# Optimization experiments

Measured on AMD Instinct MI355X. Metric: run time of the kernel, lower is better.

Reference implementation:

```python
import jax, jax.numpy as jnp
import numpy as np

N = 8192
D = 128
NUM_CLASSES = 1000
MARGIN = 1.0
EPS = 1e-6  # torch.nn.functional.pairwise_distance default eps
FMAX = float(np.finfo(np.float32).max)


def setup_inputs() -> dict:
    key = jax.random.key(0)
    k_e, k_l = jax.random.split(key)
    embed = jax.random.normal(k_e, (N, D), dtype=jnp.float32)
    labels = jax.random.randint(k_l, (N,), 0, NUM_CLASSES, dtype=jnp.int64)
    return {"embed": embed, "labels": labels}


def reference(embed, labels):
    # Pairwise squared-L2 distance matrix: ||xi||^2 - 2 xi.xj + ||xj||^2  -> [N, N]
    norm_sq = jnp.sum(embed * embed, axis=1, keepdims=True)  # [N, 1]
    dist = norm_sq - 2.0 * (embed @ embed.T) + norm_sq.T     # [N, N]

    # Label similarity mask (int in original; float here for the multiplies)
    sim = (labels[:, None] == labels[None, :]).astype(dist.dtype)  # [N, N]

    # Hardest positive: argmax of masked distances
    hardest_pos = jnp.argmax(dist * sim, axis=1)  # [N]

    # Hardest negative: argmin over negatives, sentinel-replacing masked-out entries
    neg_masked = dist * (1.0 - sim)
    hardest_neg = jnp.argmin(neg_masked + (neg_masked <= 0).astype(dist.dtype) * FMAX, axis=1)

    a = embed
    p = embed[hardest_pos]  # [N, D]
    n = embed[hardest_neg]  # [N, D]

    # torch.nn.TripletMarginLoss(margin=MARGIN): mean(relu(d(a,p) - d(a,n) + margin))
    # with d(x, y) = ||x - y + eps||_2 (torch pairwise_distance semantics)
    d_ap = jnp.sqrt(jnp.sum((a - p + EPS) ** 2, axis=1))
    d_an = jnp.sqrt(jnp.sum((a - n + EPS) ** 2, axis=1))
    loss = jnp.mean(jnp.maximum(d_ap - d_an + MARGIN, 0.0))
    return loss
```

## Files before the change

### kernel.cpp

```cpp
#include <hip/hip_runtime.h>
#include <cstdint>

typedef unsigned long long u64;
typedef _Float16 half8 __attribute__((ext_vector_type(8)));
typedef float f32x4 __attribute__((ext_vector_type(4)));

static constexpr int Dd = 128;
static constexpr float EPSf = 1e-6f;
static constexpr float MARGINf = 1.0f;
static constexpr float BIGf = 3.0e38f;

__device__ __forceinline__ unsigned fkey(float f) {
  unsigned b = __float_as_uint(f);
  return (b & 0x80000000u) ? ~b : (b | 0x80000000u);
}

__global__ __launch_bounds__(256) void k_prep(const float* __restrict__ E,
                                              _Float16* __restrict__ Ehp,
                                              float* __restrict__ normf) {
  __shared__ float part[4][16];
  const int t = threadIdx.x;
  const int b = blockIdx.x;
  const int ks = t >> 6, r15 = t & 15;
  const int lg = (t >> 4) & 3;
  const float* src = E + (size_t)(b * 16 + r15) * Dd + ks * 32 + lg * 8;
  float4 v0 = *(const float4*)src;
  float4 v1 = *(const float4*)(src + 4);
  half8 hv;
  hv[0] = (_Float16)v0.x; hv[1] = (_Float16)v0.y;
  hv[2] = (_Float16)v0.z; hv[3] = (_Float16)v0.w;
  hv[4] = (_Float16)v1.x; hv[5] = (_Float16)v1.y;
  hv[6] = (_Float16)v1.z; hv[7] = (_Float16)v1.w;
  *(half8*)((char*)Ehp + (size_t)b * 4096 + t * 16) = hv;
  float s = v0.x * v0.x + v0.y * v0.y + v0.z * v0.z + v0.w * v0.w +
            v1.x * v1.x + v1.y * v1.y + v1.z * v1.z + v1.w * v1.w;
  s += __shfl_xor(s, 16);
  s += __shfl_xor(s, 32);
  if (((t >> 4) & 3) == 0) part[ks][r15] = s;
  __syncthreads();
  if (t < 16) normf[b * 16 + t] = part[0][t] + part[1][t] + part[2][t] + part[3][t];
}

__global__ __launch_bounds__(256, 3) void k_gemm(const _Float16* __restrict__ Ehp,
                                                 const float* __restrict__ normf,
                                                 const int* __restrict__ lab,
                                                 u64* __restrict__ posPart,
                                                 u64* __restrict__ negPart) {
  __shared__ __align__(16) char Jb[2][16384];
  __shared__ __align__(16) float njs[1024];
  __shared__ __align__(16) int ljs[1024];

  const int t = threadIdx.x;
  const int w = t >> 6, l = t & 63;
  const int lane15 = l & 15, lg = l >> 4;
  const int iw = w & 1, jw = w >> 1;
  const int panel = blockIdx.x;
  const int strip = blockIdx.y;
  const int ibase = panel * 128;
  const int jbase = strip * 1024;
  const char* jsrc = (const char*)Ehp + (size_t)(jbase >> 4) * 4096;

  #pragma unroll
  for (int q = 0; q < 4; ++q)
    *(half8*)(Jb[0] + q * 4096 + t * 16) = *(const half8*)(jsrc + q * 4096 + t * 16);
  *(float4*)&njs[t * 4] = *(const float4*)&normf[jbase + t * 4];
  *(int4*)&ljs[t * 4] = *(const int4*)&lab[jbase + t * 4];

  const int gi0 = ibase + iw * 64;
  half8 bf[4][4];
  #pragma unroll
  for (int it = 0; it < 4; ++it)
    #pragma unroll
    for (int ks = 0; ks < 4; ++ks)
      bf[it][ks] = *(const half8*)(Ehp + ((size_t)((gi0 >> 4) + it) * 4 + ks) * 512 +
                                   (size_t)l * 8);
  int li[4];
  #pragma unroll
  for (int it = 0; it < 4; ++it) li[it] = lab[gi0 + it * 16 + lane15];
  __syncthreads();

  float bp[4] = {-BIGf, -BIGf, -BIGf, -BIGf};
  float bn[4] = {BIGf, BIGf, BIGf, BIGf};

  for (int tile = 0; tile < 16; ++tile) {
    const int cur = tile & 1;
    half8 sreg[4];
    if (tile < 15) {
      const char* s = jsrc + (size_t)(tile + 1) * 16384;
      #pragma unroll
      for (int q = 0; q < 4; ++q) sreg[q] = *(const half8*)(s + q * 4096 + t * 16);
    }

    f32x4 acc[2][4];
    #pragma unroll
    for (int a = 0; a < 2; ++a)
      #pragma unroll
      for (int b = 0; b < 4; ++b) acc[a][b] = (f32x4){0.f, 0.f, 0.f, 0.f};

    #pragma unroll
    for (int ks = 0; ks < 4; ++ks) {
      half8 aj[2];
      #pragma unroll
      for (int jt = 0; jt < 2; ++jt)
        aj[jt] = *(const half8*)(Jb[cur] + ((jw * 2 + jt) * 4 + ks) * 1024 + l * 16);
      __builtin_amdgcn_s_setprio(1);
      #pragma unroll
      for (int jt = 0; jt < 2; ++jt)
        #pragma unroll
        for (int it = 0; it < 4; ++it)
          acc[jt][it] = __builtin_amdgcn_mfma_f32_16x16x32_f16(aj[jt], bf[it][ks], acc[jt][it], 0, 0, 0);
      __builtin_amdgcn_s_setprio(0);
    }

    #pragma unroll
    for (int jt = 0; jt < 2; ++jt) {
      const int jr0 = tile * 64 + jw * 32 + jt * 16 + lg * 4;
      const float4 nj4 = *(const float4*)&njs[jr0];
      const int4 lj4 = *(const int4*)&ljs[jr0];
      #pragma unroll
      for (int it = 0; it < 4; ++it) {
        float c0 = fmaf(acc[jt][it][0], -2.0f, nj4.x);
        float c1 = fmaf(acc[jt][it][1], -2.0f, nj4.y);
        float c2 = fmaf(acc[jt][it][2], -2.0f, nj4.z);
        float c3 = fmaf(acc[jt][it][3], -2.0f, nj4.w);
        c0 = __uint_as_float((__float_as_uint(c0) & 0xFFFFFC00u) | (unsigned)(jr0 + 0));
        c1 = __uint_as_float((__float_as_uint(c1) & 0xFFFFFC00u) | (unsigned)(jr0 + 1));
        c2 = __uint_as_float((__float_as_uint(c2) & 0xFFFFFC00u) | (unsigned)(jr0 + 2));
        c3 = __uint_as_float((__float_as_uint(c3) & 0xFFFFFC00u) | (unsigned)(jr0 + 3));
        bool s0 = (lj4.x == li[it]), s1 = (lj4.y == li[it]);
        bool s2 = (lj4.z == li[it]), s3 = (lj4.w == li[it]);
        float p0 = s0 ? c0 : -BIGf, p1 = s1 ? c1 : -BIGf;
        float p2 = s2 ? c2 : -BIGf, p3 = s3 ? c3 : -BIGf;
        float n0 = s0 ? BIGf : c0, n1 = s1 ? BIGf : c1;
        float n2 = s2 ? BIGf : c2, n3 = s3 ? BIGf : c3;
        bp[it] = fmaxf(bp[it], fmaxf(fmaxf(p0, p1), fmaxf(p2, p3)));
        bn[it] = fminf(bn[it], fminf(fminf(n0, n1), fminf(n2, n3)));
      }
    }

    __syncthreads();
    if (tile < 15) {
      #pragma unroll
      for (int q = 0; q < 4; ++q)
        *(half8*)(Jb[cur ^ 1] + q * 4096 + t * 16) = sreg[q];
    }
    __syncthreads();
  }

  #pragma unroll
  for (int it = 0; it < 4; ++it) {
    bp[it] = fmaxf(bp[it], __shfl_xor(bp[it], 16));
    bp[it] = fmaxf(bp[it], __shfl_xor(bp[it], 32));
    bn[it] = fminf(bn[it], __shfl_xor(bn[it], 16));
    bn[it] = fminf(bn[it], __shfl_xor(bn[it], 32));
  }
  if (l < 16) {
    const int slot = strip * 2 + jw;
    #pragma unroll
    for (int it = 0; it < 4; ++it) {
      int gi = ibase + iw * 64 + it * 16 + lane15;
      unsigned gjp = (unsigned)jbase + (__float_as_uint(bp[it]) & 1023u);
      unsigned gjn = (unsigned)jbase + (__float_as_uint(bn[it]) & 1023u);
      posPart[(size_t)slot * 8192 + gi] =
          ((u64)fkey(bp[it]) << 32) | (u64)(0xFFFFFFFFu - gjp);
      negPart[(size_t)slot * 8192 + gi] = ((u64)fkey(bn[it]) << 32) | (u64)gjn;
    }
  }
}

__global__ __launch_bounds__(256) void k_final(const float* __restrict__ E,
                                               const u64* __restrict__ posPart,
                                               const u64* __restrict__ negPart,
                                               float* __restrict__ rowLoss) {
  int i = (blockIdx.x * 256 + threadIdx.x) >> 6;
  int l = threadIdx.x & 63;
  u64 pp = 0ull, np = ~0ull;
  if (l < 16) {
    pp = posPart[(size_t)l * 8192 + i];
    np = negPart[(size_t)l * 8192 + i];
  }
  #pragma unroll
  for (int off = 1; off < 64; off <<= 1) {
    u64 a = __shfl_xor(pp, off);
    u64 b = __shfl_xor(np, off);
    pp = pp > a ? pp : a;
    np = np < b ? np : b;
  }
  int jp = (int)((0xFFFFFFFFu - (unsigned)(pp & 0xFFFFFFFFull)) & 8191u);
  int jn = (int)((unsigned)(np & 0xFFFFFFFFull) & 8191u);
  float2 a = *(const float2*)(E + (size_t)i * Dd + l * 2);
  float2 p = *(const float2*)(E + (size_t)jp * Dd + l * 2);
  float2 n = *(const float2*)(E + (size_t)jn * Dd + l * 2);
  float dx = a.x - p.x + EPSf, dy = a.y - p.y + EPSf;
  float sap = dx * dx + dy * dy;
  dx = a.x - n.x + EPSf;
  dy = a.y - n.y + EPSf;
  float san = dx * dx + dy * dy;
  #pragma unroll
  for (int off = 32; off; off >>= 1) {
    sap += __shfl_xor(sap, off);
    san += __shfl_xor(san, off);
  }
  if (l == 0) rowLoss[i] = fmaxf(sqrtf(sap) - sqrtf(san) + MARGINf, 0.0f);
}

__global__ __launch_bounds__(256) void k_reduce(const float* __restrict__ rowLoss,
                                                float* __restrict__ out) {
  __shared__ float s[256];
  int t = threadIdx.x;
  float sum = 0.f;
  for (int q = 0; q < 32; ++q) sum += rowLoss[t + 256 * q];
  s[t] = sum;
  __syncthreads();
  for (int off = 128; off; off >>= 1) {
    if (t < off) s[t] += s[t + off];
    __syncthreads();
  }
  if (t == 0) out[0] = s[0] * (1.0f / 8192.0f);
}

extern "C" void kernel_launch(void* const* d_in, const int* in_sizes, int n_in,
                              void* d_out, int out_size, void* d_ws, size_t ws_size,
                              hipStream_t stream) {
  const float* E = (const float*)d_in[0];
  const int* lab = (const int*)d_in[1];
  float* out = (float*)d_out;

  char* wsp = (char*)d_ws;
  u64* posPart = (u64*)wsp;
  u64* negPart = (u64*)(wsp + (1024 << 10));
  float* normf = (float*)(wsp + (2048 << 10));
  float* rowLoss = (float*)(wsp + (2080 << 10));
  _Float16* Ehp = (_Float16*)(wsp + (2112 << 10));

  k_prep<<<512, 256, 0, stream>>>(E, Ehp, normf);
  k_gemm<<<dim3(64, 8), 256, 0, stream>>>(Ehp, normf, lab, posPart, negPart);
  k_final<<<2048, 256, 0, stream>>>(E, posPart, negPart, rowLoss);
  k_reduce<<<1, 256, 0, stream>>>(rowLoss, out);
}
```

Before: 43.53 us.

## Double waves per GEMM block, each wave covering 16 j-rows per tile

The distance/argmax GEMM block grows from 256 to 512 threads (8 waves). Each wave now handles a single 16-row j sub-tile instead of two, which halves per-wave accumulator registers and per-wave MFMA work. The intent is more latency hiding and wave-level parallelism. In exchange, the partial-result slots double to 32 per row, so the final kernel reduces 32 candidates and workspace offsets move. It also adds more redundant B-fragment register loads per block, since every wave still holds the full 64-row i fragment.

```diff
diff --git a/kernel.cpp b/kernel.cpp
--- a/kernel.cpp
+++ b/kernel.cpp
@@ -41,7 +41,7 @@
   if (t < 16) normf[b * 16 + t] = part[0][t] + part[1][t] + part[2][t] + part[3][t];
 }
 
-__global__ __launch_bounds__(256, 3) void k_gemm(const _Float16* __restrict__ Ehp,
+__global__ __launch_bounds__(512, 4) void k_gemm(const _Float16* __restrict__ Ehp,
                                                  const float* __restrict__ normf,
                                                  const int* __restrict__ lab,
                                                  u64* __restrict__ posPart,
@@ -61,10 +61,10 @@
   const char* jsrc = (const char*)Ehp + (size_t)(jbase >> 4) * 4096;
 
   #pragma unroll
-  for (int q = 0; q < 4; ++q)
-    *(half8*)(Jb[0] + q * 4096 + t * 16) = *(const half8*)(jsrc + q * 4096 + t * 16);
-  *(float4*)&njs[t * 4] = *(const float4*)&normf[jbase + t * 4];
-  *(int4*)&ljs[t * 4] = *(const int4*)&lab[jbase + t * 4];
+  for (int q = 0; q < 2; ++q)
+    *(half8*)(Jb[0] + q * 8192 + t * 16) = *(const half8*)(jsrc + q * 8192 + t * 16);
+  *(float2*)&njs[t * 2] = *(const float2*)&normf[jbase + t * 2];
+  *(int2*)&ljs[t * 2] = *(const int2*)&lab[jbase + t * 2];
 
   const int gi0 = ibase + iw * 64;
   half8 bf[4][4];
@@ -84,45 +84,37 @@
 
   for (int tile = 0; tile < 16; ++tile) {
     const int cur = tile & 1;
-    half8 sreg[4];
+    half8 sreg[2];
     if (tile < 15) {
       const char* s = jsrc + (size_t)(tile + 1) * 16384;
       #pragma unroll
-      for (int q = 0; q < 4; ++q) sreg[q] = *(const half8*)(s + q * 4096 + t * 16);
-    }
-
-    f32x4 acc[2][4];
-    #pragma unroll
-    for (int a = 0; a < 2; ++a)
-      #pragma unroll
-      for (int b = 0; b < 4; ++b) acc[a][b] = (f32x4){0.f, 0.f, 0.f, 0.f};
+      for (int q = 0; q < 2; ++q) sreg[q] = *(const half8*)(s + q * 8192 + t * 16);
+    }
+
+    f32x4 acc[4];
+    #pragma unroll
+    for (int b = 0; b < 4; ++b) acc[b] = (f32x4){0.f, 0.f, 0.f, 0.f};
 
     #pragma unroll
     for (int ks = 0; ks < 4; ++ks) {
-      half8 aj[2];
-      #pragma unroll
-      for (int jt = 0; jt < 2; ++jt)
-        aj[jt] = *(const half8*)(Jb[cur] + ((jw * 2 + jt) * 4 + ks) * 1024 + l * 16);
+      half8 aj = *(const half8*)(Jb[cur] + (jw * 4 + ks) * 1024 + l * 16);
       __builtin_amdgcn_s_setprio(1);
       #pragma unroll
-      for (int jt = 0; jt < 2; ++jt)
-        #pragma unroll
-        for (int it = 0; it < 4; ++it)
-          acc[jt][it] = __builtin_amdgcn_mfma_f32_16x16x32_f16(aj[jt], bf[it][ks], acc[jt][it], 0, 0, 0);
+      for (int it = 0; it < 4; ++it)
+        acc[it] = __builtin_amdgcn_mfma_f32_16x16x32_f16(aj, bf[it][ks], acc[it], 0, 0, 0);
       __builtin_amdgcn_s_setprio(0);
     }
 
-    #pragma unroll
-    for (int jt = 0; jt < 2; ++jt) {
-      const int jr0 = tile * 64 + jw * 32 + jt * 16 + lg * 4;
+    {
+      const int jr0 = tile * 64 + jw * 16 + lg * 4;
       const float4 nj4 = *(const float4*)&njs[jr0];
       const int4 lj4 = *(const int4*)&ljs[jr0];
       #pragma unroll
       for (int it = 0; it < 4; ++it) {
-        float c0 = fmaf(acc[jt][it][0], -2.0f, nj4.x);
-        float c1 = fmaf(acc[jt][it][1], -2.0f, nj4.y);
-        float c2 = fmaf(acc[jt][it][2], -2.0f, nj4.z);
-        float c3 = fmaf(acc[jt][it][3], -2.0f, nj4.w);
+        float c0 = fmaf(acc[it][0], -2.0f, nj4.x);
+        float c1 = fmaf(acc[it][1], -2.0f, nj4.y);
+        float c2 = fmaf(acc[it][2], -2.0f, nj4.z);
+        float c3 = fmaf(acc[it][3], -2.0f, nj4.w);
         c0 = __uint_as_float((__float_as_uint(c0) & 0xFFFFFC00u) | (unsigned)(jr0 + 0));
         c1 = __uint_as_float((__float_as_uint(c1) & 0xFFFFFC00u) | (unsigned)(jr0 + 1));
         c2 = __uint_as_float((__float_as_uint(c2) & 0xFFFFFC00u) | (unsigned)(jr0 + 2));
@@ -141,8 +133,8 @@
     __syncthreads();
     if (tile < 15) {
       #pragma unroll
-      for (int q = 0; q < 4; ++q)
-        *(half8*)(Jb[cur ^ 1] + q * 4096 + t * 16) = sreg[q];
+      for (int q = 0; q < 2; ++q)
+        *(half8*)(Jb[cur ^ 1] + q * 8192 + t * 16) = sreg[q];
     }
     __syncthreads();
   }
@@ -155,7 +147,7 @@
     bn[it] = fminf(bn[it], __shfl_xor(bn[it], 32));
   }
   if (l < 16) {
-    const int slot = strip * 2 + jw;
+    const int slot = strip * 4 + jw;
     #pragma unroll
     for (int it = 0; it < 4; ++it) {
       int gi = ibase + iw * 64 + it * 16 + lane15;
@@ -175,7 +167,7 @@
   int i = (blockIdx.x * 256 + threadIdx.x) >> 6;
   int l = threadIdx.x & 63;
   u64 pp = 0ull, np = ~0ull;
-  if (l < 16) {
+  if (l < 32) {
     pp = posPart[(size_t)l * 8192 + i];
     np = negPart[(size_t)l * 8192 + i];
   }
@@ -228,13 +220,13 @@
 
   char* wsp = (char*)d_ws;
   u64* posPart = (u64*)wsp;
-  u64* negPart = (u64*)(wsp + (1024 << 10));
-  float* normf = (float*)(wsp + (2048 << 10));
-  float* rowLoss = (float*)(wsp + (2080 << 10));
-  _Float16* Ehp = (_Float16*)(wsp + (2112 << 10));
+  u64* negPart = (u64*)(wsp + (2048 << 10));
+  float* normf = (float*)(wsp + (4096 << 10));
+  float* rowLoss = (float*)(wsp + (4128 << 10));
+  _Float16* Ehp = (_Float16*)(wsp + (4160 << 10));
 
   k_prep<<<512, 256, 0, stream>>>(E, Ehp, normf);
-  k_gemm<<<dim3(64, 8), 256, 0, stream>>>(Ehp, normf, lab, posPart, negPart);
+  k_gemm<<<dim3(64, 8), 512, 0, stream>>>(Ehp, normf, lab, posPart, negPart);
   k_final<<<2048, 256, 0, stream>>>(E, posPart, negPart, rowLoss);
   k_reduce<<<1, 256, 0, stream>>>(rowLoss, out);
 }
```

Result: slower. 48.99 us (+12.6%).
